# Kernel tuning notes

Hardware: AMD Instinct MI355X
Metric: run time of the kernel (lower is better)

Reference implementation:

```python
import jax, jax.numpy as jnp
import numpy as np

EPS = 1e-5
POOL = 4  # two stacked AvgPool3d(2) == one AvgPool3d(4, stride=4) on the valid region


def setup_inputs() -> dict:
    key = jax.random.key(0)
    k1, k2, k3 = jax.random.split(key, 3)
    N, Cin, Cout, D = 16, 32, 16, 32
    x = jax.random.normal(k1, (N, Cin, D, D, D), dtype=jnp.float32)
    w = jax.random.normal(k2, (Cin, Cout, 3, 3, 3), dtype=jnp.float32) * 0.1
    b = jax.random.normal(k3, (Cout,), dtype=jnp.float32) * 0.1
    gamma = jnp.ones((Cout,), dtype=jnp.float32)
    beta = jnp.zeros((Cout,), dtype=jnp.float32)
    return {"x": x, "w": w, "b": b, "gamma": gamma, "beta": beta}


def _convT_bn_pool(x, w, b, gamma, beta):
    # ConvTranspose3d(stride=2, padding=1, K=3) == dilated conv with
    # lhs_dilation=2, padding=K-1-p=1, spatially-flipped kernel, IO->OI swap.
    wt = jnp.flip(w, axis=(2, 3, 4)).transpose(1, 0, 2, 3, 4)  # [Cout,Cin,3,3,3]
    y = jax.lax.conv_general_dilated(
        x, wt,
        window_strides=(1, 1, 1),
        padding=[(1, 1), (1, 1), (1, 1)],
        lhs_dilation=(2, 2, 2),
        dimension_numbers=("NCDHW", "OIDHW", "NCDHW"),
    )
    y = y + b[None, :, None, None, None]  # [N,Cout,Dout,Hout,Wout], Dout=2D-1

    # BatchNorm training stats: biased variance over (N,D,H,W) per channel
    mean = jnp.mean(y, axis=(0, 2, 3, 4), keepdims=True)
    var = jnp.mean(jnp.square(y - mean), axis=(0, 2, 3, 4), keepdims=True)
    inv = jax.lax.rsqrt(var + EPS)
    yn = (y - mean) * inv * gamma[None, :, None, None, None] + beta[None, :, None, None, None]

    # Two AvgPool3d(2) == AvgPool3d(4, stride 4) on the cropped valid region
    N_, C_, Do, Ho, Wo = yn.shape
    D2, H2, W2 = Do // POOL, Ho // POOL, Wo // POOL
    yn = yn[:, :, : D2 * POOL, : H2 * POOL, : W2 * POOL]
    yn = yn.reshape(N_, C_, D2, POOL, H2, POOL, W2, POOL)
    return jnp.mean(yn, axis=(3, 5, 7))  # [N,C,D2,H2,W2]


def reference(x, w, b, gamma, beta):
    return _convT_bn_pool(x, w, b, gamma, beta)
```

## Files before the change

### kernel.cpp

```cpp
#include <hip/hip_runtime.h>


typedef __attribute__((ext_vector_type(8))) short bf16x8;
typedef __attribute__((ext_vector_type(4))) float f32x4;

static __device__ __forceinline__ unsigned short f2bf(float f) {
    unsigned int u = __float_as_uint(f);
    u = (u + 0x7fffu + ((u >> 16) & 1u)) >> 16;
    return (unsigned short)u;
}
static __device__ __forceinline__ unsigned pack2(float a, float b) {
    return (unsigned)f2bf(a) | ((unsigned)f2bf(b) << 16);
}

__global__ __launch_bounds__(256)
void kw(const float* __restrict__ w, unsigned short* __restrict__ wT)
{
    const int idx = blockIdx.x * 256 + threadIdx.x;
    if (idx < 13824) {
        const int ci = idx & 31, co = (idx >> 5) & 15, tap = idx >> 9;
        wT[idx] = f2bf(w[(ci * 16 + co) * 27 + tap]);
    }
}

__global__ __launch_bounds__(256, 3)
void convf2(const float* __restrict__ x,
            const unsigned short* __restrict__ wT,
            const float* __restrict__ bias,
            float* __restrict__ pooled,
            float* __restrict__ psum, float* __restrict__ psq)
{
    const int ht = blockIdx.x, dt = blockIdx.y, n = blockIdx.z;
    const int tid = threadIdx.x;
    const int v = tid >> 6, lane = tid & 63;
    const int t = v & 1, odp = v >> 1;
    const int c = lane & 15, qd = lane >> 4;

    __shared__ unsigned short xs[9504];
    __shared__ float sred[4][16], qred[4][16], pbuf[2][8][16];

    #pragma unroll
    for (int p = 0; p < 5; ++p) {
        const int dihi = p * 2 + (tid >> 7);
        if (dihi < 9) {
            const int iw = tid & 31, g = (tid >> 5) & 3;
            const int di = dihi / 3, hi = dihi - di * 3;
            const int id = 2*dt + di, ih = 2*ht + hi;
            const bool ok = (id < 32) && (ih < 32);
            const float* px = x + ((((n*32 + g*8)*32 + id)*32 + ih)*32) + iw;
            float f[8];
            #pragma unroll
            for (int j = 0; j < 8; ++j)
                f[j] = ok ? px[j * 32768] : 0.f;
            uint4 u;
            u.x = pack2(f[0], f[1]); u.y = pack2(f[2], f[3]);
            u.z = pack2(f[4], f[5]); u.w = pack2(f[6], f[7]);
            *(uint4*)(xs + dihi*1056 + g*264 + iw*8) = u;
        }
    }
    if (tid < 36) {
        const int dihi = tid >> 2, g = tid & 3;
        *(uint4*)(xs + dihi*1056 + g*264 + 256) = make_uint4(0,0,0,0);
    }

    auto LDBg = [&](int tap) -> bf16x8 {
        return *(const bf16x8*)(wT + tap * 512 + c * 32 + qd * 8);
    };
    bf16x8 Ba[9];
    #pragma unroll
    for (int i = 0; i < 9; ++i) Ba[i] = LDBg(9 + i);

    __syncthreads();

    f32x4 acc[2][4][2];
    #pragma unroll
    for (int ol = 0; ol < 2; ++ol)
        #pragma unroll
        for (int oh = 0; oh < 4; ++oh)
            #pragma unroll
            for (int par = 0; par < 2; ++par)
                acc[ol][oh][par] = (f32x4){0.f,0.f,0.f,0.f};

    const int iwb = 16 * t + c;
    auto LDA = [&](int dihi, int sofs) -> bf16x8 {
        return *(const bf16x8*)(xs + dihi*1056 + qd*264 + (iwb + sofs)*8);
    };

    constexpr int HN[3] = {2, 3, 1};
    constexpr int HKH[3][3] = {{1,2,0},{0,1,2},{0,0,0}};
    constexpr int HOH[3][3] = {{0,1,0},{1,2,3},{3,0,0}};

    auto PH = [&](int ol, const bf16x8* B, int di) {
        #pragma unroll
        for (int hi = 0; hi < 3; ++hi) {
            const bf16x8 A0 = LDA(di*3 + hi, 0), A1 = LDA(di*3 + hi, 1);
            #pragma unroll
            for (int j = 0; j < 3; ++j)
                if (j < HN[hi]) {
                    const int kh = HKH[hi][j], oh = HOH[hi][j];
                    acc[ol][oh][0] = __builtin_amdgcn_mfma_f32_16x16x32_bf16(
                        A0, B[kh*3 + 1], acc[ol][oh][0], 0, 0, 0);
                    acc[ol][oh][1] = __builtin_amdgcn_mfma_f32_16x16x32_bf16(
                        A1, B[kh*3 + 0], acc[ol][oh][1], 0, 0, 0);
                    acc[ol][oh][1] = __builtin_amdgcn_mfma_f32_16x16x32_bf16(
                        A0, B[kh*3 + 2], acc[ol][oh][1], 0, 0, 0);
                }
        }
    };

    PH(0, Ba, odp);
    #pragma unroll
    for (int i = 0; i < 9; ++i) Ba[i] = LDBg(18 + i);
    PH(1, Ba, odp);
    #pragma unroll
    for (int i = 0; i < 9; ++i) Ba[i] = LDBg(i);
    PH(1, Ba, odp + 1);

    const float bv = bias[c];
    float s = 0.f, sq = 0.f;
    float P[2] = {0.f, 0.f};
    #pragma unroll
    for (int ol = 0; ol < 2; ++ol) {
        const int odg = 2*odp + ol;
        const bool odok = !(dt == 15 && odg == 3);
        #pragma unroll
        for (int oh = 0; oh < 4; ++oh) {
            const bool ohok = !(ht == 15 && oh == 3);
            #pragma unroll
            for (int par = 0; par < 2; ++par)
                #pragma unroll
                for (int r = 0; r < 4; ++r) {
                    const float val = acc[ol][oh][par][r] + bv;
                    const bool owok = !(par == 1 && t == 1 && qd == 3 && r == 3);
                    const float mk = (odok && ohok && owok) ? 1.f : 0.f;
                    s += mk * val; sq += mk * val * val;
                    P[r >> 1] += val;
                }
        }
    }
    s  += __shfl_xor(s, 16, 64);  s  += __shfl_xor(s, 32, 64);
    sq += __shfl_xor(sq, 16, 64); sq += __shfl_xor(sq, 32, 64);

    if (lane < 16) { sred[v][lane] = s; qred[v][lane] = sq; }
    if (odp == 0 && dt < 15 && ht < 15) {
        pbuf[t][2*qd + 0][c] = P[0];
        pbuf[t][2*qd + 1][c] = P[1];
    }
    __syncthreads();
    if (tid < 16) {
        const int blk = (n*16 + dt)*16 + ht;
        psum[tid*4096 + blk] = sred[0][tid]+sred[1][tid]+sred[2][tid]+sred[3][tid];
        psq [tid*4096 + blk] = qred[0][tid]+qred[1][tid]+qred[2][tid]+qred[3][tid];
    }
    if (odp == 1 && dt < 15 && ht < 15) {
        #pragma unroll
        for (int jj = 0; jj < 2; ++jj) {
            const int jl = 2*qd + jj, jg = 8*t + jl;
            if (jg < 15) {
                const float tot = pbuf[t][jl][c] + P[jj];
                pooled[(n*16 + c)*3375 + dt*225 + ht*15 + jg] = tot * (1.f/64.f);
            }
        }
    }
}

__global__ void bnfinal(const float* __restrict__ psum, const float* __restrict__ psq,
                        const float* __restrict__ gamma, const float* __restrict__ beta,
                        float* __restrict__ bn)
{
    const int co = blockIdx.x;
    const int t  = threadIdx.x;
    float S = 0, Q = 0;
    for (int blk = t; blk < 4096; blk += 256) {
        S += psum[co*4096 + blk];
        Q += psq [co*4096 + blk];
    }
    #pragma unroll
    for (int off = 32; off > 0; off >>= 1) {
        S += __shfl_down(S, off, 64);
        Q += __shfl_down(Q, off, 64);
    }
    __shared__ float rs[4], rq[4];
    if ((t & 63) == 0) { rs[t >> 6] = S; rq[t >> 6] = Q; }
    __syncthreads();
    if (t == 0) {
        S = rs[0] + rs[1] + rs[2] + rs[3];
        Q = rq[0] + rq[1] + rq[2] + rq[3];
        const float cnt = 16.f * 63.f * 63.f * 63.f;
        const float mean = S / cnt;
        const float var  = Q / cnt - mean * mean;
        const float inv  = rsqrtf(var + 1e-5f);
        const float sc   = inv * gamma[co];
        bn[co]      = sc;
        bn[16 + co] = beta[co] - mean * sc;
    }
}

__global__ void finalize(const float* __restrict__ pooled, const float* __restrict__ bn,
                         float* __restrict__ out)
{
    const int i  = blockIdx.x * 256 + threadIdx.x;
    const int co = (i / 3375) & 15;
    out[i] = pooled[i] * bn[co] + bn[16 + co];
}

extern "C" void kernel_launch(void* const* d_in, const int* in_sizes, int n_in,
                              void* d_out, int out_size, void* d_ws, size_t ws_size,
                              hipStream_t stream)
{
    const float* x     = (const float*)d_in[0];
    const float* w     = (const float*)d_in[1];
    const float* b     = (const float*)d_in[2];
    const float* gamma = (const float*)d_in[3];
    const float* beta  = (const float*)d_in[4];
    float* out = (float*)d_out;

    char* wsb = (char*)d_ws;
    unsigned short* wT = (unsigned short*)wsb;
    float* pooled = (float*)(wsb + 27648);
    float* psum   = (float*)(wsb + 27648 + 3456000);
    float* psq    = (float*)(wsb + 27648 + 3456000 + 262144);
    float* bn     = (float*)(wsb + 27648 + 3456000 + 2*262144);

    kw<<<54, 256, 0, stream>>>(w, wT);
    dim3 grid(16, 16, 16);
    convf2<<<grid, 256, 0, stream>>>(x, wT, b, pooled, psum, psq);
    bnfinal<<<16, 256, 0, stream>>>(psum, psq, gamma, beta, bn);
    finalize<<<3375, 256, 0, stream>>>(pooled, bn, out);
}
```

Measured before the change: 144.2 us.

## Split conv depth tile in half to double block count and cut LDS

```diff
diff --git a/kernel.cpp b/kernel.cpp
--- a/kernel.cpp
+++ b/kernel.cpp
@@ -23,42 +23,42 @@
     }
 }
 
-__global__ __launch_bounds__(256, 3)
-void convf2(const float* __restrict__ x,
+__global__ __launch_bounds__(256, 4)
+void convf4(const float* __restrict__ x,
             const unsigned short* __restrict__ wT,
             const float* __restrict__ bias,
-            float* __restrict__ pooled,
+            float* __restrict__ pooled2,
             float* __restrict__ psum, float* __restrict__ psq)
 {
-    const int ht = blockIdx.x, dt = blockIdx.y, n = blockIdx.z;
+    const int ht = blockIdx.x, dtp = blockIdx.y, n = blockIdx.z;
     const int tid = threadIdx.x;
     const int v = tid >> 6, lane = tid & 63;
-    const int t = v & 1, odp = v >> 1;
+    const int t  = __builtin_amdgcn_readfirstlane(v & 1);
+    const int ks = __builtin_amdgcn_readfirstlane(v >> 1);
     const int c = lane & 15, qd = lane >> 4;
 
-    __shared__ unsigned short xs[9504];
+    __shared__ unsigned short xs[6336];
     __shared__ float sred[4][16], qred[4][16], pbuf[2][8][16];
 
     #pragma unroll
-    for (int p = 0; p < 5; ++p) {
-        const int dihi = p * 2 + (tid >> 7);
-        if (dihi < 9) {
-            const int iw = tid & 31, g = (tid >> 5) & 3;
-            const int di = dihi / 3, hi = dihi - di * 3;
-            const int id = 2*dt + di, ih = 2*ht + hi;
-            const bool ok = (id < 32) && (ih < 32);
-            const float* px = x + ((((n*32 + g*8)*32 + id)*32 + ih)*32) + iw;
-            float f[8];
-            #pragma unroll
-            for (int j = 0; j < 8; ++j)
-                f[j] = ok ? px[j * 32768] : 0.f;
-            uint4 u;
-            u.x = pack2(f[0], f[1]); u.y = pack2(f[2], f[3]);
-            u.z = pack2(f[4], f[5]); u.w = pack2(f[6], f[7]);
-            *(uint4*)(xs + dihi*1056 + g*264 + iw*8) = u;
-        }
-    }
-    if (tid < 36) {
+    for (int p = 0; p < 3; ++p) {
+        const int task = tid + 256 * p;
+        const int dihi = task >> 7;
+        const int iw = task & 31, g = (task >> 5) & 3;
+        const int di = dihi / 3, hi = dihi - di * 3;
+        const int id = dtp + di, ih = 2*ht + hi;
+        const bool ok = (id < 32) && (ih < 32);
+        const float* px = x + ((((n*32 + g*8)*32 + id)*32 + ih)*32) + iw;
+        float f[8];
+        #pragma unroll
+        for (int j = 0; j < 8; ++j)
+            f[j] = ok ? px[j * 32768] : 0.f;
+        uint4 u;
+        u.x = pack2(f[0], f[1]); u.y = pack2(f[2], f[3]);
+        u.z = pack2(f[4], f[5]); u.w = pack2(f[6], f[7]);
+        *(uint4*)(xs + dihi*1056 + g*264 + iw*8) = u;
+    }
+    if (tid < 24) {
         const int dihi = tid >> 2, g = tid & 3;
         *(uint4*)(xs + dihi*1056 + g*264 + 256) = make_uint4(0,0,0,0);
     }
@@ -66,20 +66,19 @@
     auto LDBg = [&](int tap) -> bf16x8 {
         return *(const bf16x8*)(wT + tap * 512 + c * 32 + qd * 8);
     };
-    bf16x8 Ba[9];
-    #pragma unroll
-    for (int i = 0; i < 9; ++i) Ba[i] = LDBg(9 + i);
+    bf16x8 Bf[9];
+    const int kdA = ks ? 2 : 1;
+    #pragma unroll
+    for (int i = 0; i < 9; ++i) Bf[i] = LDBg(kdA*9 + i);
 
     __syncthreads();
 
-    f32x4 acc[2][4][2];
-    #pragma unroll
-    for (int ol = 0; ol < 2; ++ol)
-        #pragma unroll
-        for (int oh = 0; oh < 4; ++oh)
-            #pragma unroll
-            for (int par = 0; par < 2; ++par)
-                acc[ol][oh][par] = (f32x4){0.f,0.f,0.f,0.f};
+    f32x4 acc[4][2];
+    #pragma unroll
+    for (int oh = 0; oh < 4; ++oh)
+        #pragma unroll
+        for (int par = 0; par < 2; ++par)
+            acc[oh][par] = (f32x4){0.f,0.f,0.f,0.f};
 
     const int iwb = 16 * t + c;
     auto LDA = [&](int dihi, int sofs) -> bf16x8 {
@@ -90,7 +89,7 @@
     constexpr int HKH[3][3] = {{1,2,0},{0,1,2},{0,0,0}};
     constexpr int HOH[3][3] = {{0,1,0},{1,2,3},{3,0,0}};
 
-    auto PH = [&](int ol, const bf16x8* B, int di) {
+    auto PH = [&](int di) {
         #pragma unroll
         for (int hi = 0; hi < 3; ++hi) {
             const bf16x8 A0 = LDA(di*3 + hi, 0), A1 = LDA(di*3 + hi, 1);
@@ -98,68 +97,64 @@
             for (int j = 0; j < 3; ++j)
                 if (j < HN[hi]) {
                     const int kh = HKH[hi][j], oh = HOH[hi][j];
-                    acc[ol][oh][0] = __builtin_amdgcn_mfma_f32_16x16x32_bf16(
-                        A0, B[kh*3 + 1], acc[ol][oh][0], 0, 0, 0);
-                    acc[ol][oh][1] = __builtin_amdgcn_mfma_f32_16x16x32_bf16(
-                        A1, B[kh*3 + 0], acc[ol][oh][1], 0, 0, 0);
-                    acc[ol][oh][1] = __builtin_amdgcn_mfma_f32_16x16x32_bf16(
-                        A0, B[kh*3 + 2], acc[ol][oh][1], 0, 0, 0);
+                    acc[oh][0] = __builtin_amdgcn_mfma_f32_16x16x32_bf16(
+                        A0, Bf[kh*3 + 1], acc[oh][0], 0, 0, 0);
+                    acc[oh][1] = __builtin_amdgcn_mfma_f32_16x16x32_bf16(
+                        A1, Bf[kh*3 + 0], acc[oh][1], 0, 0, 0);
+                    acc[oh][1] = __builtin_amdgcn_mfma_f32_16x16x32_bf16(
+                        A0, Bf[kh*3 + 2], acc[oh][1], 0, 0, 0);
                 }
         }
     };
 
-    PH(0, Ba, odp);
-    #pragma unroll
-    for (int i = 0; i < 9; ++i) Ba[i] = LDBg(18 + i);
-    PH(1, Ba, odp);
-    #pragma unroll
-    for (int i = 0; i < 9; ++i) Ba[i] = LDBg(i);
-    PH(1, Ba, odp + 1);
-
+    PH(0);
+    if (ks) {
+        #pragma unroll
+        for (int i = 0; i < 9; ++i) Bf[i] = LDBg(i);
+        PH(1);
+    }
+
+    const bool odok = (2*dtp + ks) < 63;
     const float bv = bias[c];
     float s = 0.f, sq = 0.f;
     float P[2] = {0.f, 0.f};
     #pragma unroll
-    for (int ol = 0; ol < 2; ++ol) {
-        const int odg = 2*odp + ol;
-        const bool odok = !(dt == 15 && odg == 3);
-        #pragma unroll
-        for (int oh = 0; oh < 4; ++oh) {
-            const bool ohok = !(ht == 15 && oh == 3);
+    for (int oh = 0; oh < 4; ++oh) {
+        const bool ohok = !(ht == 15 && oh == 3);
+        #pragma unroll
+        for (int par = 0; par < 2; ++par)
             #pragma unroll
-            for (int par = 0; par < 2; ++par)
-                #pragma unroll
-                for (int r = 0; r < 4; ++r) {
-                    const float val = acc[ol][oh][par][r] + bv;
-                    const bool owok = !(par == 1 && t == 1 && qd == 3 && r == 3);
-                    const float mk = (odok && ohok && owok) ? 1.f : 0.f;
-                    s += mk * val; sq += mk * val * val;
-                    P[r >> 1] += val;
-                }
-        }
+            for (int r = 0; r < 4; ++r) {
+                const float val = acc[oh][par][r] + bv;
+                const bool owok = !(par == 1 && t == 1 && qd == 3 && r == 3);
+                const float mk = (odok && ohok && owok) ? 1.f : 0.f;
+                s += mk * val; sq += mk * val * val;
+                P[r >> 1] += val;
+            }
     }
     s  += __shfl_xor(s, 16, 64);  s  += __shfl_xor(s, 32, 64);
     sq += __shfl_xor(sq, 16, 64); sq += __shfl_xor(sq, 32, 64);
 
+    const int dq = dtp >> 1, half = dtp & 1;
+    const bool pok = (dq < 15) && (ht < 15);
     if (lane < 16) { sred[v][lane] = s; qred[v][lane] = sq; }
-    if (odp == 0 && dt < 15 && ht < 15) {
+    if (ks == 0 && pok) {
         pbuf[t][2*qd + 0][c] = P[0];
         pbuf[t][2*qd + 1][c] = P[1];
     }
     __syncthreads();
     if (tid < 16) {
-        const int blk = (n*16 + dt)*16 + ht;
-        psum[tid*4096 + blk] = sred[0][tid]+sred[1][tid]+sred[2][tid]+sred[3][tid];
-        psq [tid*4096 + blk] = qred[0][tid]+qred[1][tid]+qred[2][tid]+qred[3][tid];
-    }
-    if (odp == 1 && dt < 15 && ht < 15) {
+        const int blk = (n*32 + dtp)*16 + ht;
+        psum[tid*8192 + blk] = sred[0][tid]+sred[1][tid]+sred[2][tid]+sred[3][tid];
+        psq [tid*8192 + blk] = qred[0][tid]+qred[1][tid]+qred[2][tid]+qred[3][tid];
+    }
+    if (ks == 1 && pok) {
         #pragma unroll
         for (int jj = 0; jj < 2; ++jj) {
             const int jl = 2*qd + jj, jg = 8*t + jl;
-            if (jg < 15) {
-                const float tot = pbuf[t][jl][c] + P[jj];
-                pooled[(n*16 + c)*3375 + dt*225 + ht*15 + jg] = tot * (1.f/64.f);
-            }
+            if (jg < 15)
+                pooled2[half*864000 + (n*16 + c)*3375 + dq*225 + ht*15 + jg] =
+                    pbuf[t][jl][c] + P[jj];
         }
     }
 }
@@ -171,9 +166,9 @@
     const int co = blockIdx.x;
     const int t  = threadIdx.x;
     float S = 0, Q = 0;
-    for (int blk = t; blk < 4096; blk += 256) {
-        S += psum[co*4096 + blk];
-        Q += psq [co*4096 + blk];
+    for (int blk = t; blk < 8192; blk += 256) {
+        S += psum[co*8192 + blk];
+        Q += psq [co*8192 + blk];
     }
     #pragma unroll
     for (int off = 32; off > 0; off >>= 1) {
@@ -196,12 +191,13 @@
     }
 }
 
-__global__ void finalize(const float* __restrict__ pooled, const float* __restrict__ bn,
+__global__ void finalize(const float* __restrict__ pooled2, const float* __restrict__ bn,
                          float* __restrict__ out)
 {
     const int i  = blockIdx.x * 256 + threadIdx.x;
     const int co = (i / 3375) & 15;
-    out[i] = pooled[i] * bn[co] + bn[16 + co];
+    const float tot = pooled2[i] + pooled2[864000 + i];
+    out[i] = tot * (1.f/64.f) * bn[co] + bn[16 + co];
 }
 
 extern "C" void kernel_launch(void* const* d_in, const int* in_sizes, int n_in,
@@ -217,14 +213,14 @@
 
     char* wsb = (char*)d_ws;
     unsigned short* wT = (unsigned short*)wsb;
-    float* pooled = (float*)(wsb + 27648);
-    float* psum   = (float*)(wsb + 27648 + 3456000);
-    float* psq    = (float*)(wsb + 27648 + 3456000 + 262144);
-    float* bn     = (float*)(wsb + 27648 + 3456000 + 2*262144);
+    float* pooled2 = (float*)(wsb + 27648);
+    float* psum    = (float*)(wsb + 27648 + 6912000);
+    float* psq     = (float*)(wsb + 27648 + 6912000 + 524288);
+    float* bn      = (float*)(wsb + 27648 + 6912000 + 2*524288);
 
     kw<<<54, 256, 0, stream>>>(w, wT);
-    dim3 grid(16, 16, 16);
-    convf2<<<grid, 256, 0, stream>>>(x, wT, b, pooled, psum, psq);
+    dim3 grid(16, 32, 16);
+    convf4<<<grid, 256, 0, stream>>>(x, wT, b, pooled2, psum, psq);
     bnfinal<<<16, 256, 0, stream>>>(psum, psq, gamma, beta, bn);
-    finalize<<<3375, 256, 0, stream>>>(pooled, bn, out);
-}
+    finalize<<<3375, 256, 0, stream>>>(pooled2, bn, out);
+}
```

Result: slower. 148.0 us (+2.6%).
